# Performance work log

Measured on AMD Instinct MI355X. Metric: run time of the kernel, lower is better.

Reference implementation:

```python
import jax, jax.numpy as jnp
import numpy as np

N, E = 50000, 800000
IN_C, OUT_C, HEADS = 128, 16, 8
EDGE_DIM = 1
NEG_SLOPE = 0.2
LN_EPS = 1e-5


def setup_inputs() -> dict:
    key = jax.random.key(0)
    ks = jax.random.split(key, 12)
    s = 1.0 / np.sqrt(IN_C)
    HC = OUT_C * HEADS
    return {
        "x": jax.random.normal(ks[0], (N, IN_C), jnp.float32),
        "edge_index": jax.random.randint(ks[1], (2, E), 0, N, jnp.int32),
        "edge_attr": jax.random.normal(ks[2], (E, EDGE_DIM), jnp.float32),
        "W": jax.random.normal(ks[3], (IN_C, HC), jnp.float32) * s,
        "b": jnp.zeros((HC,), jnp.float32),
        "att_src": jax.random.normal(ks[4], (HEADS, OUT_C), jnp.float32) * s,
        "att_dst": jax.random.normal(ks[5], (HEADS, OUT_C), jnp.float32) * s,
        "att_edge": jax.random.normal(ks[6], (HEADS, OUT_C), jnp.float32) * s,
        "lin_edge_w": jax.random.normal(ks[7], (EDGE_DIM, HC), jnp.float32) * s,
        "lin_edge_b": jnp.zeros((HC,), jnp.float32),
        "gamma": jnp.ones((HC,), jnp.float32),
        "beta": jnp.zeros((HC,), jnp.float32),
    }


def _segment_softmax(logits, seg, num_segments):
    # numerically-stable softmax over edges grouped by destination node
    m = jax.ops.segment_max(logits, seg, num_segments=num_segments)
    ex = jnp.exp(logits - m[seg])
    z = jax.ops.segment_sum(ex, seg, num_segments=num_segments)
    return ex / (z[seg] + 1e-16)


def reference(x, edge_index, edge_attr, W, b, att_src, att_dst, att_edge,
              lin_edge_w, lin_edge_b, gamma, beta):
    n = x.shape[0]
    src, dst = edge_index[0], edge_index[1]
    # GAT conv: per-head transform, edge-indexed attention, segment softmax, scatter-add
    h = (x @ W).reshape(n, HEADS, OUT_C)                      # [N,H,C]
    a_src = jnp.einsum('nhc,hc->nh', h, att_src)              # [N,H]
    a_dst = jnp.einsum('nhc,hc->nh', h, att_dst)
    e = (edge_attr @ lin_edge_w + lin_edge_b).reshape(-1, HEADS, OUT_C)
    a_edge = jnp.einsum('ehc,hc->eh', e, att_edge)            # [E,H]
    logits = jax.nn.leaky_relu(a_src[src] + a_dst[dst] + a_edge, NEG_SLOPE)
    alpha = _segment_softmax(logits, dst, n)                  # [E,H]
    msg = alpha[..., None] * h[src]                           # [E,H,C]
    out = jax.ops.segment_sum(msg, dst, num_segments=n).reshape(n, -1) + b
    # residual (in_channels == heads*out_channels -> identity projection)
    out = out + x
    # LayerNorm + ELU (dropout is eval-mode identity)
    mu = jnp.mean(out, axis=-1, keepdims=True)
    var = jnp.var(out, axis=-1, keepdims=True)
    out = (out - mu) * jax.lax.rsqrt(var + LN_EPS) * gamma + beta
    return jax.nn.elu(out)
```

## Files before the change

kernel.cpp:

```cpp
#include <hip/hip_runtime.h>
#include <hip/hip_bf16.h>

#define N_NODES 50000
#define N_EDGES 800000
#define IN_C 128
#define HC 128
#define HEADS 8
#define NEG_SLOPE 0.2f
#define LN_EPS 1e-5f

#define LDH 136
#define ELL_CAP 64
#define GEMM_BLOCKS 782
#define FILL_BLOCKS 782
#define FUSED_BLOCKS (GEMM_BLOCKS + FILL_BLOCKS)
#define NBUCK 392
#define BCAP 8
#define OVF_CAP 8192
#define SENT 0xFFFFFFFFFFFFFFFFull

typedef __hip_bfloat16 bf16;
typedef __attribute__((ext_vector_type(8))) short short8;
typedef __attribute__((ext_vector_type(4))) float f32x4;
typedef unsigned long long u64;

__device__ __forceinline__ float b2f(bf16 v) { return __bfloat162float(v); }

__device__ __forceinline__ unsigned short f2bf(float f) {
    unsigned u = __float_as_uint(f);
    return (unsigned short)((u + 0x7fffu + ((u >> 16) & 1u)) >> 16);
}
__device__ __forceinline__ float bf2f(unsigned s) {
    return __uint_as_float(s << 16);
}
__device__ __forceinline__ short8 pack8(float4 u, float4 v) {
    short8 r;
    r[0] = (short)f2bf(u.x); r[1] = (short)f2bf(u.y);
    r[2] = (short)f2bf(u.z); r[3] = (short)f2bf(u.w);
    r[4] = (short)f2bf(v.x); r[5] = (short)f2bf(v.y);
    r[6] = (short)f2bf(v.z); r[7] = (short)f2bf(v.w);
    return r;
}

union FusedSm {
    short sH[4][16 * LDH];
    struct {
        u64 recs[NBUCK][BCAP];
        int lcnt[NBUCK];
    } bin;
};

__global__ __launch_bounds__(256) void prep(
    const float* __restrict__ W, unsigned short* __restrict__ Wt,
    int* __restrict__ ovfc)
{
    int id = blockIdx.x * 256 + threadIdx.x;
    int k = id >> 7, n = id & 127;
    Wt[n * 128 + k] = f2bf(W[id]);
    if (id == 0) *ovfc = 0;
}

__device__ __forceinline__ void gemm_body(
    int gid, int t,
    const float* __restrict__ x, const unsigned short* __restrict__ Wt,
    const float* __restrict__ att_src, const float* __restrict__ att_dst,
    unsigned short* __restrict__ h_out,
    float* __restrict__ a_src, float* __restrict__ a_dst,
    short (*sH)[16 * LDH])
{
    const int wv  = t >> 6;
    const int l   = t & 63;
    const int gw  = gid * 4 + wv;
    if (gw >= N_NODES / 16) return;

    const int n0   = gw * 16;
    const int mrow = l & 15;
    const int quad = l >> 4;

    short8 afrag[4];
    const float* xr = x + (size_t)(n0 + mrow) * IN_C + quad * 8;
#pragma unroll
    for (int ko = 0; ko < 4; ++ko) {
        float4 u = *reinterpret_cast<const float4*>(xr + ko * 32);
        float4 v = *reinterpret_cast<const float4*>(xr + ko * 32 + 4);
        afrag[ko] = pack8(u, v);
    }

    f32x4 acc[8];
#pragma unroll
    for (int nt = 0; nt < 8; ++nt) acc[nt] = (f32x4)0.f;
#pragma unroll
    for (int nt = 0; nt < 8; ++nt) {
        const unsigned short* wr = Wt + (nt * 16 + mrow) * 128 + quad * 8;
#pragma unroll
        for (int ko = 0; ko < 4; ++ko) {
            short8 bfr = *reinterpret_cast<const short8*>(wr + ko * 32);
            acc[nt] = __builtin_amdgcn_mfma_f32_16x16x32_bf16(afrag[ko], bfr, acc[nt], 0, 0, 0);
        }
    }

#pragma unroll
    for (int nt = 0; nt < 8; ++nt)
#pragma unroll
        for (int r = 0; r < 4; ++r)
            sH[wv][(quad * 4 + r) * LDH + nt * 16 + mrow] = (short)f2bf(acc[nt][r]);

#pragma unroll
    for (int i = 0; i < 4; ++i) {
        int row = i * 4 + (l >> 4);
        int col = (l & 15) * 8;
        short8 hv = *reinterpret_cast<const short8*>(&sH[wv][row * LDH + col]);
        *reinterpret_cast<short8*>(h_out + (size_t)(n0 + row) * HC + col) = hv;
    }

#pragma unroll
    for (int pp = 0; pp < 2; ++pp) {
        int p  = l + pp * 64;
        int m  = p >> 3;
        int hd = p & 7;
        float ssum = 0.f, dsum = 0.f;
#pragma unroll
        for (int c = 0; c < 16; ++c) {
            float hv = bf2f((unsigned short)sH[wv][m * LDH + hd * 16 + c]);
            ssum = fmaf(hv, att_src[hd * 16 + c], ssum);
            dsum = fmaf(hv, att_dst[hd * 16 + c], dsum);
        }
        a_src[(n0 + m) * HEADS + hd] = ssum;
        a_dst[(n0 + m) * HEADS + hd] = dsum;
    }
}

__global__ __launch_bounds__(256) void fused(
    const float* __restrict__ x, const unsigned short* __restrict__ Wt,
    const float* __restrict__ att_src, const float* __restrict__ att_dst,
    const int* __restrict__ ei, const float* __restrict__ edge_attr,
    u64* __restrict__ arena, int* __restrict__ ovfc, u64* __restrict__ ovf,
    unsigned short* __restrict__ h_out,
    float* __restrict__ a_src, float* __restrict__ a_dst)
{
    __shared__ FusedSm sm;
    const int bid = blockIdx.x;
    const int t   = threadIdx.x;

    if (bid & 1) {
        const int blk = bid >> 1;
        for (int i = t; i < NBUCK; i += 256) sm.bin.lcnt[i] = 0;
        __syncthreads();

        const int e0 = blk * 1024 + t * 4;
        if (e0 < N_EDGES) {
            const int4   s4 = *reinterpret_cast<const int4*>(ei + e0);
            const int4   d4 = *reinterpret_cast<const int4*>(ei + N_EDGES + e0);
            const float4 a4 = *reinterpret_cast<const float4*>(edge_attr + e0);
#define BIN1(D, S, A)                                                      \
            {                                                              \
                const unsigned w_ =                                        \
                    (((unsigned)(S)) << 16) | (unsigned)f2bf(A);           \
                const int b_ = (D) >> 7;                                   \
                int p_ = atomicAdd(&sm.bin.lcnt[b_], 1);                   \
                if (p_ < BCAP)                                             \
                    sm.bin.recs[b_][p_] =                                  \
                        ((u64)(unsigned)((D) & 127) << 32) | (u64)w_;      \
                else {                                                     \
                    int op_ = atomicAdd(ovfc, 1);                          \
                    if (op_ < OVF_CAP)                                     \
                        ovf[op_] = ((u64)(unsigned)(D) << 32) | (u64)w_;   \
                }                                                          \
            }
            BIN1(d4.x, s4.x, a4.x)
            BIN1(d4.y, s4.y, a4.y)
            BIN1(d4.z, s4.z, a4.z)
            BIN1(d4.w, s4.w, a4.w)
#undef BIN1
        }
        __syncthreads();
        for (int i = t; i < NBUCK * BCAP; i += 256) {
            const int bi = i >> 3;
            const int j  = i & 7;
            u64 v = (j < sm.bin.lcnt[bi]) ? sm.bin.recs[bi][j] : SENT;
            arena[((size_t)bi * FILL_BLOCKS + blk) * BCAP + j] = v;
        }
        return;
    }

    gemm_body(bid >> 1, t, x, Wt, att_src, att_dst, h_out, a_src, a_dst, sm.sH);
}

__global__ __launch_bounds__(512) void ebuild(
    const u64* __restrict__ arena, const int* __restrict__ ovfc,
    const u64* __restrict__ ovf,
    unsigned int* __restrict__ ellp, int* __restrict__ cnt)
{
    __shared__ unsigned int ell[128 * ELL_CAP];
    __shared__ int lc[128];
    const int t = threadIdx.x;
    const int b = blockIdx.x;
    if (t < 128) lc[t] = 0;
    __syncthreads();

    const u64* seg = arena + (size_t)b * (FILL_BLOCKS * BCAP);
    for (int q = t; q < FILL_BLOCKS * BCAP; q += 512) {
        const u64 rec = seg[q];
        if (rec != SENT) {
            const int dl = (int)(rec >> 32);
            int p = atomicAdd(&lc[dl], 1);
            if (p < ELL_CAP) ell[(dl << 6) + p] = (unsigned)rec;
        }
    }
    const int ovn = min(*ovfc, OVF_CAP);
    for (int q = t; q < ovn; q += 512) {
        const u64 rec = ovf[q];
        const int n = (int)(rec >> 32);
        if ((n >> 7) == b) {
            int p = atomicAdd(&lc[n & 127], 1);
            if (p < ELL_CAP) ell[((n & 127) << 6) + p] = (unsigned)rec;
        }
    }
    __syncthreads();
    uint4* eg = reinterpret_cast<uint4*>(ellp + ((size_t)b << 13));
    const uint4* es = reinterpret_cast<const uint4*>(ell);
#pragma unroll
    for (int q = t; q < 128 * ELL_CAP / 4; q += 512) eg[q] = es[q];
    if (t < 128) {
        const int n = (b << 7) + t;
        if (n < N_NODES) cnt[n] = min(lc[t], ELL_CAP);
    }
}


#define LROW(CE, HV, J, OFF, B0)                                           \
    { int cj_ = __builtin_amdgcn_ds_swizzle((int)(CE), OFF);               \
      size_t r_ = ((B0) + (J) < cn) ? (size_t)(((unsigned)cj_) >> 16) : 0; \
      (HV)[J] = h2[r_ * 64 + l]; }
#define LOADROWS(CE, HV, B0)                                               \
    LROW(CE, HV, 0,  24, B0) LROW(CE, HV, 1,  56, B0)                      \
    LROW(CE, HV, 2,  88, B0) LROW(CE, HV, 3, 120, B0)                      \
    LROW(CE, HV, 4, 152, B0) LROW(CE, HV, 5, 184, B0)                      \
    LROW(CE, HV, 6, 216, B0) LROW(CE, HV, 7, 248, B0)

#define FROW(EV, HV, J, OFF)                                               \
    { float evj_ = __uint_as_float((unsigned)__builtin_amdgcn_ds_swizzle(  \
          __float_as_int(EV), OFF));                                       \
      acc0 = fmaf(evj_, b2f((HV)[J].x), acc0);                             \
      acc1 = fmaf(evj_, b2f((HV)[J].y), acc1); }
#define FMAROWS(EV, HV)                                                    \
    FROW(EV, HV, 0,  24) FROW(EV, HV, 1,  56) FROW(EV, HV, 2,  88)        \
    FROW(EV, HV, 3, 120) FROW(EV, HV, 4, 152) FROW(EV, HV, 5, 184)        \
    FROW(EV, HV, 6, 216) FROW(EV, HV, 7, 248)

__global__ __launch_bounds__(256) void gather_node(
    const int* __restrict__ cnt, const unsigned int* __restrict__ ellp,
    const float* __restrict__ a_src, const float* __restrict__ a_dst,
    const bf16* __restrict__ h,
    const float* __restrict__ x, const float* __restrict__ bvec,
    const float* __restrict__ gamma, const float* __restrict__ beta,
    const float* __restrict__ att_edge, const float* __restrict__ lin_w,
    const float* __restrict__ lin_b,
    float* __restrict__ out)
{
    const int wave = threadIdx.x >> 6;
    const int l    = threadIdx.x & 63;
    const int n    = blockIdx.x * 4 + wave;
    const int hh   = l >> 3;
    const int jj   = l & 7;

    float ae0 = att_edge[2 * l], ae1 = att_edge[2 * l + 1];
    float p = ae0 * lin_w[2 * l] + ae1 * lin_w[2 * l + 1];
    float q = ae0 * lin_b[2 * l] + ae1 * lin_b[2 * l + 1];
#pragma unroll
    for (int off = 1; off <= 4; off <<= 1) {
        p += __shfl_xor(p, off, 64);
        q += __shfl_xor(q, off, 64);
    }
    const float2 bv = *reinterpret_cast<const float2*>(bvec + 2 * l);
    const float2 gv = *reinterpret_cast<const float2*>(gamma + 2 * l);
    const float2 be = *reinterpret_cast<const float2*>(beta + 2 * l);

    const float adq = a_dst[n * HEADS + hh] + q;
    const int   beg = n << 6;
    const int   cn  = min(cnt[n], ELL_CAP);

    float zp = 0.f, acc0 = 0.f, acc1 = 0.f;
    const __hip_bfloat162* h2 = reinterpret_cast<const __hip_bfloat162*>(h);

    if (cn > 0) {
        unsigned ce_c = ellp[beg + jj];
        float    as_c = a_src[(ce_c >> 16) * HEADS + hh];
        __hip_bfloat162 hv_c[8], hv_n[8];
        LOADROWS(ce_c, hv_c, 0)

        for (int bs = 0; ; bs += 8) {
            const unsigned ce   = ce_c;
            const float    as   = as_c;
            const bool     last = (bs + 8 >= cn);
            if (!last) {
                ce_c = ellp[beg + bs + 8 + jj];
                LOADROWS(ce_c, hv_n, bs + 8)
                as_c = a_src[(ce_c >> 16) * HEADS + hh];
            }
            const float ea = bf2f(ce & 0xffffu);
            float lg = fmaf(ea, p, as + adq);
            lg = fmaxf(lg, NEG_SLOPE * lg);
            const float ev = (bs + jj < cn) ? __expf(lg) : 0.f;
            zp += ev;
            FMAROWS(ev, hv_c)
            if (last) break;
#pragma unroll
            for (int j = 0; j < 8; ++j) hv_c[j] = hv_n[j];
        }
    }

    float z = zp;
    z += __shfl_xor(z, 1, 64);
    z += __shfl_xor(z, 2, 64);
    z += __shfl_xor(z, 4, 64);
    const float rz = 1.f / (z + 1e-16f);
    acc0 *= rz;
    acc1 *= rz;

    const size_t idx = (size_t)n * HC + 2 * l;
    const float2 xv = *reinterpret_cast<const float2*>(x + idx);
    float v0 = acc0 + xv.x + bv.x;
    float v1 = acc1 + xv.y + bv.y;
    float s1 = v0 + v1, s2 = v0 * v0 + v1 * v1;
#pragma unroll
    for (int off = 32; off >= 1; off >>= 1) {
        s1 += __shfl_xor(s1, off, 64);
        s2 += __shfl_xor(s2, off, 64);
    }
    const float mean = s1 * (1.f / HC);
    const float var  = s2 * (1.f / HC) - mean * mean;
    const float inv  = rsqrtf(var + LN_EPS);
    float y0 = (v0 - mean) * inv * gv.x + be.x;
    float y1 = (v1 - mean) * inv * gv.y + be.y;
    y0 = y0 > 0.f ? y0 : expm1f(y0);
    y1 = y1 > 0.f ? y1 : expm1f(y1);
    *reinterpret_cast<float2*>(out + idx) = make_float2(y0, y1);
}

extern "C" void kernel_launch(void* const* d_in, const int* in_sizes, int n_in,
                              void* d_out, int out_size, void* d_ws, size_t ws_size,
                              hipStream_t stream)
{
    const float* x         = (const float*)d_in[0];
    const int*   ei        = (const int*)d_in[1];
    const float* edge_attr = (const float*)d_in[2];
    const float* W         = (const float*)d_in[3];
    const float* b         = (const float*)d_in[4];
    const float* att_src   = (const float*)d_in[5];
    const float* att_dst   = (const float*)d_in[6];
    const float* att_edge  = (const float*)d_in[7];
    const float* lin_w     = (const float*)d_in[8];
    const float* lin_b     = (const float*)d_in[9];
    const float* gamma     = (const float*)d_in[10];
    const float* beta      = (const float*)d_in[11];

    char* ws = (char*)d_ws;
    bf16*  h     = (bf16*)ws;  ws += (size_t)N_NODES * HC * sizeof(bf16);
    float* a_src = (float*)ws; ws += (size_t)N_NODES * HEADS * sizeof(float);
    float* a_dst = (float*)ws; ws += (size_t)N_NODES * HEADS * sizeof(float);
    int*   cnt   = (int*)ws;   ws += (size_t)N_NODES * sizeof(int);
    unsigned short* Wt = (unsigned short*)ws;
    ws += (size_t)128 * 128 * sizeof(unsigned short);
    unsigned int* ellp = (unsigned int*)ws;
    ws += (size_t)(NBUCK * 128 * ELL_CAP + 64) * sizeof(unsigned int);
    int* ovfc = (int*)ws;      ws += 64;
    u64* ovf  = (u64*)ws;      ws += (size_t)OVF_CAP * sizeof(u64);
    u64* arena = (u64*)d_out;

    prep<<<64, 256, 0, stream>>>(W, Wt, ovfc);

    fused<<<FUSED_BLOCKS, 256, 0, stream>>>(
        x, Wt, att_src, att_dst, ei, edge_attr, arena, ovfc, ovf,
        (unsigned short*)h, a_src, a_dst);

    ebuild<<<NBUCK, 512, 0, stream>>>(arena, ovfc, ovf, ellp, cnt);

    gather_node<<<N_NODES / 4, 256, 0, stream>>>(
        cnt, ellp, a_src, a_dst, h, x, b, gamma, beta,
        att_edge, lin_w, lin_b, (float*)d_out);
}
```

Before: 186.5 us.

## Split edge binning into two bucket passes and transpose arena layout

The fill blocks now bin edges in two passes over half the buckets each, which halves the shared-memory footprint of the binning struct (recs+lcnt). That could let the fused kernel use less LDS if the GEMM union member is not the larger one. The arena is transposed to block-major, so each fill block writes one contiguous stretch, while ebuild now reads strided 64-byte chunks across blocks. The cost is an extra pass with more barriers, and each edge is tested twice.

```diff
diff --git a/kernel.cpp b/kernel.cpp
--- a/kernel.cpp
+++ b/kernel.cpp
@@ -15,6 +15,7 @@
 #define FILL_BLOCKS 782
 #define FUSED_BLOCKS (GEMM_BLOCKS + FILL_BLOCKS)
 #define NBUCK 392
+#define HBUCK 196
 #define BCAP 8
 #define OVF_CAP 8192
 #define SENT 0xFFFFFFFFFFFFFFFFull
@@ -45,8 +46,8 @@
 union FusedSm {
     short sH[4][16 * LDH];
     struct {
-        u64 recs[NBUCK][BCAP];
-        int lcnt[NBUCK];
+        u64 recs[HBUCK][BCAP];
+        int lcnt[HBUCK];
     } bin;
 };
 
@@ -144,41 +145,54 @@
 
     if (bid & 1) {
         const int blk = bid >> 1;
-        for (int i = t; i < NBUCK; i += 256) sm.bin.lcnt[i] = 0;
-        __syncthreads();
-
-        const int e0 = blk * 1024 + t * 4;
-        if (e0 < N_EDGES) {
-            const int4   s4 = *reinterpret_cast<const int4*>(ei + e0);
-            const int4   d4 = *reinterpret_cast<const int4*>(ei + N_EDGES + e0);
-            const float4 a4 = *reinterpret_cast<const float4*>(edge_attr + e0);
+        const int e0  = blk * 1024 + t * 4;
+        const bool val = (e0 < N_EDGES);
+        int4 s4 = {0,0,0,0}, d4 = {0,0,0,0};
+        float4 a4 = {0.f,0.f,0.f,0.f};
+        if (val) {
+            s4 = *reinterpret_cast<const int4*>(ei + e0);
+            d4 = *reinterpret_cast<const int4*>(ei + N_EDGES + e0);
+            a4 = *reinterpret_cast<const float4*>(edge_attr + e0);
+        }
+
+        for (int pass = 0; pass < 2; ++pass) {
+            const int lo = pass * HBUCK;
+            for (int i = t; i < HBUCK; i += 256) sm.bin.lcnt[i] = 0;
+            __syncthreads();
+
+            if (val) {
 #define BIN1(D, S, A)                                                      \
-            {                                                              \
-                const unsigned w_ =                                        \
-                    (((unsigned)(S)) << 16) | (unsigned)f2bf(A);           \
-                const int b_ = (D) >> 7;                                   \
-                int p_ = atomicAdd(&sm.bin.lcnt[b_], 1);                   \
-                if (p_ < BCAP)                                             \
-                    sm.bin.recs[b_][p_] =                                  \
-                        ((u64)(unsigned)((D) & 127) << 32) | (u64)w_;      \
-                else {                                                     \
-                    int op_ = atomicAdd(ovfc, 1);                          \
-                    if (op_ < OVF_CAP)                                     \
-                        ovf[op_] = ((u64)(unsigned)(D) << 32) | (u64)w_;   \
-                }                                                          \
+                {                                                          \
+                    const int b_ = (D) >> 7;                               \
+                    const unsigned lb_ = (unsigned)(b_ - lo);              \
+                    if (lb_ < HBUCK) {                                     \
+                        const unsigned w_ =                                \
+                            (((unsigned)(S)) << 16) | (unsigned)f2bf(A);   \
+                        int p_ = atomicAdd(&sm.bin.lcnt[lb_], 1);          \
+                        if (p_ < BCAP)                                     \
+                            sm.bin.recs[lb_][p_] =                         \
+                                ((u64)(unsigned)((D) & 127) << 32) | (u64)w_; \
+                        else {                                             \
+                            int op_ = atomicAdd(ovfc, 1);                  \
+                            if (op_ < OVF_CAP)                             \
+                                ovf[op_] = ((u64)(unsigned)(D) << 32) | (u64)w_; \
+                        }                                                  \
+                    }                                                      \
+                }
+                BIN1(d4.x, s4.x, a4.x)
+                BIN1(d4.y, s4.y, a4.y)
+                BIN1(d4.z, s4.z, a4.z)
+                BIN1(d4.w, s4.w, a4.w)
+#undef BIN1
             }
-            BIN1(d4.x, s4.x, a4.x)
-            BIN1(d4.y, s4.y, a4.y)
-            BIN1(d4.z, s4.z, a4.z)
-            BIN1(d4.w, s4.w, a4.w)
-#undef BIN1
-        }
-        __syncthreads();
-        for (int i = t; i < NBUCK * BCAP; i += 256) {
-            const int bi = i >> 3;
-            const int j  = i & 7;
-            u64 v = (j < sm.bin.lcnt[bi]) ? sm.bin.recs[bi][j] : SENT;
-            arena[((size_t)bi * FILL_BLOCKS + blk) * BCAP + j] = v;
+            __syncthreads();
+            for (int i = t; i < HBUCK * BCAP; i += 256) {
+                const int bi = i >> 3;
+                const int j  = i & 7;
+                u64 v = (j < sm.bin.lcnt[bi]) ? sm.bin.recs[bi][j] : SENT;
+                arena[((size_t)blk * NBUCK + lo + bi) * BCAP + j] = v;
+            }
+            __syncthreads();
         }
         return;
     }
@@ -198,9 +212,10 @@
     if (t < 128) lc[t] = 0;
     __syncthreads();
 
-    const u64* seg = arena + (size_t)b * (FILL_BLOCKS * BCAP);
     for (int q = t; q < FILL_BLOCKS * BCAP; q += 512) {
-        const u64 rec = seg[q];
+        const int blk = q >> 3;
+        const int j   = q & 7;
+        const u64 rec = arena[((size_t)blk * NBUCK + b) * BCAP + j];
         if (rec != SENT) {
             const int dl = (int)(rec >> 32);
             int p = atomicAdd(&lc[dl], 1);
```

Result: no change. 186.8 us (+0.1%).
